# Kernel tuning notes

Measured on AMD Instinct MI355X. Metric: run time of the kernel, lower is better.

## Reference

```python
import jax, jax.numpy as jnp
import numpy as np

N = 2048      # nodes per graph
Q = 9         # output_dim (emotion nodes)
D = 256       # input_dim == hidden_dim
L = 4         # num_layers - 1 GIN layers
B = 32        # batch
E = 32768     # edges per graph
EPS = 1e-5    # BatchNorm eps


def _bn(x, g, b, m, v):
    # eval-mode BatchNorm1d over last (channel) dim
    return (x - m) * (g * jax.lax.rsqrt(v + EPS)) + b


def setup_inputs() -> dict:
    key = jax.random.key(0)
    ks = jax.random.split(key, 18)
    s = 1.0 / np.sqrt(D)
    return {
        "batch_feature": jax.random.normal(ks[0], (B, N, D), jnp.float32),
        "edge_mat": jax.random.randint(ks[1], (2, E), 0, N, dtype=jnp.int32),
        "emotion_emb": jax.random.normal(ks[2], (1, Q, D), jnp.float32) * 0.05,
        "mlp_w1": jax.random.normal(ks[3], (L, D, D), jnp.float32) * s,
        "mlp_b1": jnp.zeros((L, D), jnp.float32),
        "mlp_bn_g": jnp.ones((L, D), jnp.float32),
        "mlp_bn_b": jnp.zeros((L, D), jnp.float32),
        "mlp_bn_m": jax.random.normal(ks[4], (L, D), jnp.float32) * 0.1,
        "mlp_bn_v": jax.random.uniform(ks[5], (L, D), jnp.float32, 0.5, 1.5),
        "mlp_w2": jax.random.normal(ks[6], (L, D, D), jnp.float32) * s,
        "mlp_b2": jnp.zeros((L, D), jnp.float32),
        "bn_g": jnp.ones((L, D), jnp.float32),
        "bn_b": jnp.zeros((L, D), jnp.float32),
        "bn_m": jax.random.normal(ks[7], (L, D), jnp.float32) * 0.1,
        "bn_v": jax.random.uniform(ks[8], (L, D), jnp.float32, 0.5, 1.5),
        "pred_w": jax.random.normal(ks[9], (L + 1, D), jnp.float32) * s,
        "pred_b": jnp.zeros((L + 1,), jnp.float32),
    }


def reference(batch_feature, edge_mat, emotion_emb, mlp_w1, mlp_b1,
              mlp_bn_g, mlp_bn_b, mlp_bn_m, mlp_bn_v, mlp_w2, mlp_b2,
              bn_g, bn_b, bn_m, bn_v, pred_w, pred_b):
    # overwrite first Q node rows with shared emotion embeddings
    h = batch_feature.at[:, :Q, :].set(emotion_emb)          # [B, N, D]
    src, dst = edge_mat[0], edge_mat[1]

    def spmm(x):
        # Adj @ x with self-loops; graph topology shared across batch.
        gathered = x[:, dst, :]                              # [B, E, D]
        agg = jax.vmap(
            lambda g: jax.ops.segment_sum(g, src, num_segments=N)
        )(gathered)                                          # [B, N, D]
        return agg + x  # self-loop (identity added to adjacency)

    hidden = [h]
    for l in range(L):
        pooled = spmm(h)
        # 2-layer GIN MLP: Linear -> BN -> ReLU -> Linear
        t = jnp.einsum('bnd,de->bne', pooled, mlp_w1[l]) + mlp_b1[l]
        t = jax.nn.relu(_bn(t, mlp_bn_g[l], mlp_bn_b[l], mlp_bn_m[l], mlp_bn_v[l]))
        t = jnp.einsum('bnd,de->bne', t, mlp_w2[l]) + mlp_b2[l]
        # outer BatchNorm + ReLU
        h = jax.nn.relu(_bn(t, bn_g[l], bn_b[l], bn_m[l], bn_v[l]))
        hidden.append(h)

    score = jnp.zeros((B, Q), jnp.float32)
    for l, hl in enumerate(hidden):
        h_emotion = hl[:, :Q, :]                             # [B, Q, D]
        score = score + jnp.einsum('bqd,d->bq', h_emotion, pred_w[l]) + pred_b[l]
    return jax.nn.sigmoid(score)                             # [B, Q]
```

## Files before the change

kernel.cpp:

```cpp
#include <hip/hip_runtime.h>
#include <hip/hip_bf16.h>

#define NN 2048
#define QQ 9
#define DD 256
#define LL 4
#define BB 32
#define EE 32768
#define EPSV 1e-5f

typedef __attribute__((ext_vector_type(8))) short bf16x8;
typedef __attribute__((ext_vector_type(8))) ushort u16x8;
typedef __attribute__((ext_vector_type(4))) float f32x4;
typedef __attribute__((ext_vector_type(4))) int i32x4;

__device__ __forceinline__ ushort f2bf(float x)
{
    uint u = __float_as_uint(x);
    u += 0x7FFFu + ((u >> 16) & 1u);
    return (ushort)(u >> 16);
}
__device__ __forceinline__ float bf2f(ushort h)
{
    return __uint_as_float(((uint)h) << 16);
}

__global__ void k_count(const int* __restrict__ src, int* __restrict__ cnt)
{
    int e = blockIdx.x * blockDim.x + threadIdx.x;
    if (e < EE) atomicAdd(&cnt[src[e]], 1);
}

__global__ __launch_bounds__(256) void k_scan(const int* __restrict__ cnt,
                                              int* __restrict__ row_ptr,
                                              int* __restrict__ cursor)
{
    __shared__ int part[256];
    int t = threadIdx.x;
    int local[8];
    int s = 0;
    #pragma unroll
    for (int i = 0; i < 8; ++i) { local[i] = cnt[t * 8 + i]; s += local[i]; }
    part[t] = s;
    __syncthreads();
    for (int off = 1; off < 256; off <<= 1) {
        int v = (t >= off) ? part[t - off] : 0;
        __syncthreads();
        part[t] += v;
        __syncthreads();
    }
    int run = part[t] - s;
    #pragma unroll
    for (int i = 0; i < 8; ++i) {
        int idx = t * 8 + i;
        row_ptr[idx] = run;
        cursor[idx]  = run;
        run += local[i];
    }
    if (t == 255) row_ptr[NN] = run;
}

__global__ void k_fill(const int* __restrict__ src, const int* __restrict__ dst,
                       int* __restrict__ cursor, int* __restrict__ col)
{
    int e = blockIdx.x * blockDim.x + threadIdx.x;
    if (e < EE) {
        int p = atomicAdd(&cursor[src[e]], 1);
        col[p] = dst[e];
    }
}

__global__ void k_prep0(const float4* __restrict__ bf, const float4* __restrict__ emo,
                        ushort4* __restrict__ hhi)
{
    int total = BB * NN * (DD / 4);
    for (int idx = blockIdx.x * blockDim.x + threadIdx.x; idx < total;
         idx += gridDim.x * blockDim.x) {
        int d4 = idx & 63;
        int n  = (idx >> 6) & (NN - 1);
        float4 v = (n < QQ) ? emo[n * 64 + d4] : bf[idx];
        ushort4 h;
        h.x = f2bf(v.x); h.y = f2bf(v.y); h.z = f2bf(v.z); h.w = f2bf(v.w);
        hhi[idx] = h;
    }
}

__global__ __launch_bounds__(256) void k_spmm6(
    const ushort* __restrict__ phi,
    const int* __restrict__ row_ptr, const int* __restrict__ col,
    ushort* __restrict__ ohi)
{
    int x     = blockIdx.x & 7;
    int local = blockIdx.x >> 3;
    int w     = threadIdx.x >> 6;
    int t     = threadIdx.x & 63;
    int inst  = local * 4 + w;
    int pl    = inst >> 11;
    int n     = inst & (NN - 1);
    int b     = x * 4 + pl * 2 + (t >> 5);
    int q     = t & 31;
    const ushort* base = phi + (size_t)b * NN * DD + q * 8;

    u16x8 sv = *(const u16x8*)(base + (size_t)n * DD);
    float a[8];
    #pragma unroll
    for (int k = 0; k < 8; ++k) a[k] = bf2f((ushort)sv[k]);

    int beg = row_ptr[n], end = row_ptr[n + 1];
    int j = beg;
    for (; j < end && (j & 3); ++j) {
        u16x8 g = *(const u16x8*)(base + (size_t)col[j] * DD);
        #pragma unroll
        for (int k = 0; k < 8; ++k) a[k] += bf2f((ushort)g[k]);
    }
    for (; j + 8 <= end; j += 8) {
        i32x4 c0 = *(const i32x4*)(col + j);
        i32x4 c1 = *(const i32x4*)(col + j + 4);
        u16x8 g[8];
        g[0] = *(const u16x8*)(base + (size_t)c0.x * DD);
        g[1] = *(const u16x8*)(base + (size_t)c0.y * DD);
        g[2] = *(const u16x8*)(base + (size_t)c0.z * DD);
        g[3] = *(const u16x8*)(base + (size_t)c0.w * DD);
        g[4] = *(const u16x8*)(base + (size_t)c1.x * DD);
        g[5] = *(const u16x8*)(base + (size_t)c1.y * DD);
        g[6] = *(const u16x8*)(base + (size_t)c1.z * DD);
        g[7] = *(const u16x8*)(base + (size_t)c1.w * DD);
        #pragma unroll
        for (int u = 0; u < 8; ++u)
            #pragma unroll
            for (int k = 0; k < 8; ++k) a[k] += bf2f((ushort)g[u][k]);
    }
    if (j + 4 <= end) {
        i32x4 c = *(const i32x4*)(col + j);
        u16x8 g[4];
        g[0] = *(const u16x8*)(base + (size_t)c.x * DD);
        g[1] = *(const u16x8*)(base + (size_t)c.y * DD);
        g[2] = *(const u16x8*)(base + (size_t)c.z * DD);
        g[3] = *(const u16x8*)(base + (size_t)c.w * DD);
        #pragma unroll
        for (int u = 0; u < 4; ++u)
            #pragma unroll
            for (int k = 0; k < 8; ++k) a[k] += bf2f((ushort)g[u][k]);
        j += 4;
    }
    for (; j < end; ++j) {
        u16x8 g = *(const u16x8*)(base + (size_t)col[j] * DD);
        #pragma unroll
        for (int k = 0; k < 8; ++k) a[k] += bf2f((ushort)g[k]);
    }

    u16x8 o;
    #pragma unroll
    for (int k = 0; k < 8; ++k) o[k] = f2bf(a[k]);
    *(u16x8*)(ohi + ((size_t)b * NN + n) * DD + q * 8) = o;
}

__global__ __launch_bounds__(256) void k_wprep(const float* __restrict__ w1,
                                               const float* __restrict__ w2,
                                               ushort* __restrict__ wt_hi)
{
    __shared__ float tile[32][36];
    int bx = blockIdx.x;
    int mat = bx >> 6;
    int tt  = bx & 63;
    int tk = (tt >> 3) * 32;
    int tn = (tt & 7) * 32;
    const float* src = (mat < 4) ? (w1 + (size_t)mat * DD * DD)
                                 : (w2 + (size_t)(mat - 4) * DD * DD);
    int t = threadIdx.x;
    int r = t >> 3, c0 = (t & 7) * 4;
    float4 v = *(const float4*)(src + (size_t)(tk + r) * DD + tn + c0);
    tile[r][c0 + 0] = v.x; tile[r][c0 + 1] = v.y;
    tile[r][c0 + 2] = v.z; tile[r][c0 + 3] = v.w;
    __syncthreads();
    int nn = t >> 3, kq = (t & 7) * 4;
    ushort4 hh;
    hh.x = f2bf(tile[kq + 0][nn]); hh.y = f2bf(tile[kq + 1][nn]);
    hh.z = f2bf(tile[kq + 2][nn]); hh.w = f2bf(tile[kq + 3][nn]);
    size_t off = (size_t)mat * DD * DD + (size_t)(tn + nn) * DD + tk + kq;
    *(ushort4*)(wt_hi + off) = hh;
}

__global__ __launch_bounds__(256, 2) void k_gemm_fused(
    const ushort* __restrict__ A, const ushort* __restrict__ W1t,
    const ushort* __restrict__ W2t,
    const float* __restrict__ b1, const float* __restrict__ g1,
    const float* __restrict__ be1, const float* __restrict__ m1,
    const float* __restrict__ v1,
    const float* __restrict__ b2, const float* __restrict__ g2,
    const float* __restrict__ be2, const float* __restrict__ m2,
    const float* __restrict__ v2,
    const float* __restrict__ pw, const float* __restrict__ pb, int l,
    ushort* __restrict__ O, float* __restrict__ out)
{
    __shared__ alignas(16) ushort As[2][64 * 32];
    __shared__ alignas(16) ushort Ws[2][256 * 32];
    __shared__ alignas(16) ushort Ts[64][264];

    int tid = threadIdx.x;
    int x  = blockIdx.x & 7;
    int lm = blockIdx.x >> 3;
    int m0 = x * 8192 + lm * 64;
    int lane = tid & 63;
    int w = tid >> 6;
    int wm = w & 1, wn = w >> 1;
    int lr = lane & 15, kg = lane >> 4;
    int rg = lane >> 4;

    int ar = tid >> 2, ak = (tid & 3) * 8;
    const ushort* Ab = A + (size_t)(m0 + ar) * DD + ak;

    f32x4 acc[2][8];
    #pragma unroll
    for (int m = 0; m < 2; ++m)
        #pragma unroll
        for (int n = 0; n < 8; ++n) acc[m][n] = (f32x4)0.f;

    float4 rA;
    float4 rW[4];
    rA = *(const float4*)(Ab);
    #pragma unroll
    for (int i = 0; i < 4; ++i) {
        int idx = tid + i * 256;
        int r = idx >> 2, k8 = (idx & 3) * 8;
        rW[i] = *(const float4*)(W1t + (size_t)r * DD + k8);
    }
    int cur = 0;
    for (int kc = 0; kc < 8; ++kc) {
        *(float4*)&As[cur][ar * 32 + ak] = rA;
        #pragma unroll
        for (int i = 0; i < 4; ++i) {
            int idx = tid + i * 256;
            int r = idx >> 2, k8 = (idx & 3) * 8;
            *(float4*)&Ws[cur][r * 32 + k8] = rW[i];
        }
        __syncthreads();
        if (kc < 7) {
            int k0n = (kc + 1) * 32;
            rA = *(const float4*)(Ab + k0n);
            #pragma unroll
            for (int i = 0; i < 4; ++i) {
                int idx = tid + i * 256;
                int r = idx >> 2, k8 = (idx & 3) * 8;
                rW[i] = *(const float4*)(W1t + (size_t)r * DD + k0n + k8);
            }
        }
        bf16x8 ah[2], bh[8];
        #pragma unroll
        for (int m = 0; m < 2; ++m)
            ah[m] = *(const bf16x8*)&As[cur][(wm * 32 + m * 16 + lr) * 32 + kg * 8];
        #pragma unroll
        for (int n = 0; n < 8; ++n)
            bh[n] = *(const bf16x8*)&Ws[cur][(wn * 128 + n * 16 + lr) * 32 + kg * 8];
        #pragma unroll
        for (int m = 0; m < 2; ++m)
            #pragma unroll
            for (int n = 0; n < 8; ++n)
                acc[m][n] = __builtin_amdgcn_mfma_f32_16x16x32_bf16(ah[m], bh[n], acc[m][n], 0, 0, 0);
        cur ^= 1;
    }
    {
        float sN[8], svN[8];
        #pragma unroll
        for (int n = 0; n < 8; ++n) {
            int jj = wn * 128 + n * 16 + lr;
            sN[n]  = g1[jj] * rsqrtf(v1[jj] + EPSV);
            svN[n] = (b1[jj] - m1[jj]) * sN[n] + be1[jj];
        }
        #pragma unroll
        for (int m = 0; m < 2; ++m)
            #pragma unroll
            for (int n = 0; n < 8; ++n) {
                int cc = wn * 128 + n * 16 + lr;
                #pragma unroll
                for (int r = 0; r < 4; ++r) {
                    float y = acc[m][n][r] * sN[n] + svN[n];
                    Ts[wm * 32 + m * 16 + rg * 4 + r][cc] = f2bf(y > 0.f ? y : 0.f);
                }
            }
    }
    #pragma unroll
    for (int m = 0; m < 2; ++m)
        #pragma unroll
        for (int n = 0; n < 8; ++n) acc[m][n] = (f32x4)0.f;

    __syncthreads();

    #pragma unroll
    for (int i = 0; i < 4; ++i) {
        int idx = tid + i * 256;
        int r = idx >> 2, k8 = (idx & 3) * 8;
        rW[i] = *(const float4*)(W2t + (size_t)r * DD + k8);
    }
    cur = 0;
    for (int kc = 0; kc < 8; ++kc) {
        #pragma unroll
        for (int i = 0; i < 4; ++i) {
            int idx = tid + i * 256;
            int r = idx >> 2, k8 = (idx & 3) * 8;
            *(float4*)&Ws[cur][r * 32 + k8] = rW[i];
        }
        __syncthreads();
        if (kc < 7) {
            int k0n = (kc + 1) * 32;
            #pragma unroll
            for (int i = 0; i < 4; ++i) {
                int idx = tid + i * 256;
                int r = idx >> 2, k8 = (idx & 3) * 8;
                rW[i] = *(const float4*)(W2t + (size_t)r * DD + k0n + k8);
            }
        }
        bf16x8 ah[2], bh[8];
        #pragma unroll
        for (int m = 0; m < 2; ++m)
            ah[m] = *(const bf16x8*)&Ts[wm * 32 + m * 16 + lr][kc * 32 + kg * 8];
        #pragma unroll
        for (int n = 0; n < 8; ++n)
            bh[n] = *(const bf16x8*)&Ws[cur][(wn * 128 + n * 16 + lr) * 32 + kg * 8];
        #pragma unroll
        for (int m = 0; m < 2; ++m)
            #pragma unroll
            for (int n = 0; n < 8; ++n)
                acc[m][n] = __builtin_amdgcn_mfma_f32_16x16x32_bf16(ah[m], bh[n], acc[m][n], 0, 0, 0);
        cur ^= 1;
    }
    __syncthreads();

    {
        float sN[8], svN[8];
        #pragma unroll
        for (int n = 0; n < 8; ++n) {
            int jj = wn * 128 + n * 16 + lr;
            sN[n]  = g2[jj] * rsqrtf(v2[jj] + EPSV);
            svN[n] = (b2[jj] - m2[jj]) * sN[n] + be2[jj];
        }
        #pragma unroll
        for (int m = 0; m < 2; ++m)
            #pragma unroll
            for (int n = 0; n < 8; ++n) {
                int cc = wn * 128 + n * 16 + lr;
                #pragma unroll
                for (int r = 0; r < 4; ++r) {
                    float y = acc[m][n][r] * sN[n] + svN[n];
                    Ts[wm * 32 + m * 16 + rg * 4 + r][cc] = f2bf(y > 0.f ? y : 0.f);
                }
            }
        #pragma unroll
        for (int i = 0; i < 8; ++i) {
            int cid = lane + i * 64;
            int row = cid >> 4, c8 = cid & 15;
            u16x8 vv = *(const u16x8*)&Ts[wm * 32 + row][wn * 128 + c8 * 8];
            *(u16x8*)(O + (size_t)(m0 + wm * 32 + row) * DD + wn * 128 + c8 * 8) = vv;
        }
    }

    __syncthreads();
    if ((m0 & (NN - 1)) == 0) {
        int b = m0 >> 11;
        for (int q = w; q < QQ; q += 4) {
            ushort4 hv = *(const ushort4*)&Ts[q][lane * 4];
            const float4 wv = *(const float4*)&pw[(l + 1) * DD + lane * 4];
            float s = bf2f(hv.x) * wv.x + bf2f(hv.y) * wv.y +
                      bf2f(hv.z) * wv.z + bf2f(hv.w) * wv.w;
            #pragma unroll
            for (int off = 32; off > 0; off >>= 1) s += __shfl_down(s, off);
            if (lane == 0) {
                float v = out[b * QQ + q] + s + pb[l + 1];
                out[b * QQ + q] = (l == LL - 1) ? 1.f / (1.f + expf(-v)) : v;
            }
        }
    }
}

__global__ __launch_bounds__(64) void k_score0(const float4* __restrict__ emo,
                                               const float4* __restrict__ pw,
                                               const float* __restrict__ pb,
                                               float* __restrict__ out)
{
    int q = blockIdx.x, t = threadIdx.x;
    float4 e = emo[q * 64 + t], wv = pw[t];
    float s = e.x * wv.x + e.y * wv.y + e.z * wv.z + e.w * wv.w;
    #pragma unroll
    for (int off = 32; off > 0; off >>= 1) s += __shfl_down(s, off);
    if (t == 0) {
        s += pb[0];
        for (int b = 0; b < BB; ++b) out[b * QQ + q] = s;
    }
}

extern "C" void kernel_launch(void* const* d_in, const int* in_sizes, int n_in,
                              void* d_out, int out_size, void* d_ws, size_t ws_size,
                              hipStream_t stream)
{
    const float* batch = (const float*)d_in[0];
    const int*   edges = (const int*)d_in[1];
    const float* emo   = (const float*)d_in[2];
    const float* w1    = (const float*)d_in[3];
    const float* b1    = (const float*)d_in[4];
    const float* m_g   = (const float*)d_in[5];
    const float* m_b   = (const float*)d_in[6];
    const float* m_m   = (const float*)d_in[7];
    const float* m_v   = (const float*)d_in[8];
    const float* w2    = (const float*)d_in[9];
    const float* b2    = (const float*)d_in[10];
    const float* g_g   = (const float*)d_in[11];
    const float* g_b   = (const float*)d_in[12];
    const float* g_m   = (const float*)d_in[13];
    const float* g_v   = (const float*)d_in[14];
    const float* pw    = (const float*)d_in[15];
    const float* pb    = (const float*)d_in[16];
    float* out = (float*)d_out;

    const size_t HSZ = (size_t)BB * NN * DD;
    const size_t WT  = (size_t)8 * DD * DD;

    ushort* h_hi = (ushort*)d_ws;
    ushort* P_hi = h_hi + HSZ;
    ushort* wt_hi = P_hi + HSZ;
    int* cnt     = (int*)(wt_hi + WT);
    int* row_ptr = cnt + NN;
    int* cursor  = row_ptr + (NN + 4);
    int* col     = cursor + NN;

    const int* src = edges;
    const int* dst = edges + EE;

    hipMemsetAsync(cnt, 0, NN * sizeof(int), stream);
    k_count<<<EE / 256, 256, 0, stream>>>(src, cnt);
    k_scan<<<1, 256, 0, stream>>>(cnt, row_ptr, cursor);
    k_fill<<<EE / 256, 256, 0, stream>>>(src, dst, cursor, col);
    k_wprep<<<512, 256, 0, stream>>>(w1, w2, wt_hi);
    k_prep0<<<4096, 256, 0, stream>>>((const float4*)batch, (const float4*)emo,
                                      (ushort4*)h_hi);
    k_score0<<<QQ, 64, 0, stream>>>((const float4*)emo, (const float4*)pw, pb, out);

    for (int l = 0; l < LL; ++l) {
        k_spmm6<<<8192, 256, 0, stream>>>(h_hi, row_ptr, col, P_hi);
        k_gemm_fused<<<1024, 256, 0, stream>>>(
            P_hi,
            wt_hi + (size_t)l * DD * DD, wt_hi + (size_t)(4 + l) * DD * DD,
            b1 + l * DD, m_g + l * DD, m_b + l * DD, m_m + l * DD, m_v + l * DD,
            b2 + l * DD, g_g + l * DD, g_b + l * DD, g_m + l * DD, g_v + l * DD,
            pw, pb, l,
            h_hi, out);
    }
}
```

Measured before the change: 316.7 us.

## Load GEMM operands directly from global into MFMA registers, dropping LDS staging

The fused two-GEMM kernel no longer stages A and weight tiles through double-buffered shared memory. Each wave now loads its MFMA fragments straight from global memory into register double buffers, which removes the per-k-step __syncthreads and the LDS writes and reads. In exchange, each weight tile is fetched separately by every wave that needs it instead of once per block, so L2/global traffic rises. Register pressure also grows, and the launch-bounds occupancy hint of 2 is dropped.

```diff
diff --git a/kernel.cpp b/kernel.cpp
--- a/kernel.cpp
+++ b/kernel.cpp
@@ -181,7 +181,7 @@
     *(ushort4*)(wt_hi + off) = hh;
 }
 
-__global__ __launch_bounds__(256, 2) void k_gemm_fused(
+__global__ __launch_bounds__(256) void k_gemm_fused(
     const ushort* __restrict__ A, const ushort* __restrict__ W1t,
     const ushort* __restrict__ W2t,
     const float* __restrict__ b1, const float* __restrict__ g1,
@@ -193,8 +193,6 @@
     const float* __restrict__ pw, const float* __restrict__ pb, int l,
     ushort* __restrict__ O, float* __restrict__ out)
 {
-    __shared__ alignas(16) ushort As[2][64 * 32];
-    __shared__ alignas(16) ushort Ws[2][256 * 32];
     __shared__ alignas(16) ushort Ts[64][264];
 
     int tid = threadIdx.x;
@@ -207,57 +205,36 @@
     int lr = lane & 15, kg = lane >> 4;
     int rg = lane >> 4;
 
-    int ar = tid >> 2, ak = (tid & 3) * 8;
-    const ushort* Ab = A + (size_t)(m0 + ar) * DD + ak;
-
     f32x4 acc[2][8];
     #pragma unroll
     for (int m = 0; m < 2; ++m)
         #pragma unroll
         for (int n = 0; n < 8; ++n) acc[m][n] = (f32x4)0.f;
 
-    float4 rA;
-    float4 rW[4];
-    rA = *(const float4*)(Ab);
-    #pragma unroll
-    for (int i = 0; i < 4; ++i) {
-        int idx = tid + i * 256;
-        int r = idx >> 2, k8 = (idx & 3) * 8;
-        rW[i] = *(const float4*)(W1t + (size_t)r * DD + k8);
-    }
-    int cur = 0;
+    const ushort* Ab = A + (size_t)(m0 + wm * 32 + lr) * DD + kg * 8;
+    const ushort* Wb = W1t + (size_t)(wn * 128 + lr) * DD + kg * 8;
+    bf16x8 aa[2][2], bb[2][8];
+    #pragma unroll
+    for (int mi = 0; mi < 2; ++mi) aa[0][mi] = *(const bf16x8*)(Ab + mi * 16 * DD);
+    #pragma unroll
+    for (int n = 0; n < 8; ++n)    bb[0][n]  = *(const bf16x8*)(Wb + n * 16 * DD);
+    #pragma unroll
     for (int kc = 0; kc < 8; ++kc) {
-        *(float4*)&As[cur][ar * 32 + ak] = rA;
-        #pragma unroll
-        for (int i = 0; i < 4; ++i) {
-            int idx = tid + i * 256;
-            int r = idx >> 2, k8 = (idx & 3) * 8;
-            *(float4*)&Ws[cur][r * 32 + k8] = rW[i];
-        }
-        __syncthreads();
+        const int cb = kc & 1, nb = cb ^ 1;
         if (kc < 7) {
-            int k0n = (kc + 1) * 32;
-            rA = *(const float4*)(Ab + k0n);
-            #pragma unroll
-            for (int i = 0; i < 4; ++i) {
-                int idx = tid + i * 256;
-                int r = idx >> 2, k8 = (idx & 3) * 8;
-                rW[i] = *(const float4*)(W1t + (size_t)r * DD + k0n + k8);
-            }
-        }
-        bf16x8 ah[2], bh[8];
-        #pragma unroll
-        for (int m = 0; m < 2; ++m)
-            ah[m] = *(const bf16x8*)&As[cur][(wm * 32 + m * 16 + lr) * 32 + kg * 8];
-        #pragma unroll
-        for (int n = 0; n < 8; ++n)
-            bh[n] = *(const bf16x8*)&Ws[cur][(wn * 128 + n * 16 + lr) * 32 + kg * 8];
-        #pragma unroll
-        for (int m = 0; m < 2; ++m)
+            #pragma unroll
+            for (int mi = 0; mi < 2; ++mi)
+                aa[nb][mi] = *(const bf16x8*)(Ab + mi * 16 * DD + (kc + 1) * 32);
             #pragma unroll
             for (int n = 0; n < 8; ++n)
-                acc[m][n] = __builtin_amdgcn_mfma_f32_16x16x32_bf16(ah[m], bh[n], acc[m][n], 0, 0, 0);
-        cur ^= 1;
+                bb[nb][n] = *(const bf16x8*)(Wb + n * 16 * DD + (kc + 1) * 32);
+        }
+        #pragma unroll
+        for (int mi = 0; mi < 2; ++mi)
+            #pragma unroll
+            for (int n = 0; n < 8; ++n)
+                acc[mi][n] = __builtin_amdgcn_mfma_f32_16x16x32_bf16(
+                    aa[cb][mi], bb[cb][n], acc[mi][n], 0, 0, 0);
     }
     {
         float sN[8], svN[8];
@@ -286,43 +263,27 @@
 
     __syncthreads();
 
-    #pragma unroll
-    for (int i = 0; i < 4; ++i) {
-        int idx = tid + i * 256;
-        int r = idx >> 2, k8 = (idx & 3) * 8;
-        rW[i] = *(const float4*)(W2t + (size_t)r * DD + k8);
-    }
-    cur = 0;
+    Wb = W2t + (size_t)(wn * 128 + lr) * DD + kg * 8;
+    #pragma unroll
+    for (int n = 0; n < 8; ++n) bb[0][n] = *(const bf16x8*)(Wb + n * 16 * DD);
+    #pragma unroll
     for (int kc = 0; kc < 8; ++kc) {
-        #pragma unroll
-        for (int i = 0; i < 4; ++i) {
-            int idx = tid + i * 256;
-            int r = idx >> 2, k8 = (idx & 3) * 8;
-            *(float4*)&Ws[cur][r * 32 + k8] = rW[i];
-        }
-        __syncthreads();
+        const int cb = kc & 1, nb = cb ^ 1;
         if (kc < 7) {
-            int k0n = (kc + 1) * 32;
-            #pragma unroll
-            for (int i = 0; i < 4; ++i) {
-                int idx = tid + i * 256;
-                int r = idx >> 2, k8 = (idx & 3) * 8;
-                rW[i] = *(const float4*)(W2t + (size_t)r * DD + k0n + k8);
-            }
-        }
-        bf16x8 ah[2], bh[8];
-        #pragma unroll
-        for (int m = 0; m < 2; ++m)
-            ah[m] = *(const bf16x8*)&Ts[wm * 32 + m * 16 + lr][kc * 32 + kg * 8];
-        #pragma unroll
-        for (int n = 0; n < 8; ++n)
-            bh[n] = *(const bf16x8*)&Ws[cur][(wn * 128 + n * 16 + lr) * 32 + kg * 8];
-        #pragma unroll
-        for (int m = 0; m < 2; ++m)
             #pragma unroll
             for (int n = 0; n < 8; ++n)
-                acc[m][n] = __builtin_amdgcn_mfma_f32_16x16x32_bf16(ah[m], bh[n], acc[m][n], 0, 0, 0);
-        cur ^= 1;
+                bb[nb][n] = *(const bf16x8*)(Wb + n * 16 * DD + (kc + 1) * 32);
+        }
+        bf16x8 a2[2];
+        #pragma unroll
+        for (int mi = 0; mi < 2; ++mi)
+            a2[mi] = *(const bf16x8*)&Ts[wm * 32 + mi * 16 + lr][kc * 32 + kg * 8];
+        #pragma unroll
+        for (int mi = 0; mi < 2; ++mi)
+            #pragma unroll
+            for (int n = 0; n < 8; ++n)
+                acc[mi][n] = __builtin_amdgcn_mfma_f32_16x16x32_bf16(
+                    a2[mi], bb[cb][n], acc[mi][n], 0, 0, 0);
     }
     __syncthreads();
 
```

After: 470.2 us. 48.5% more time.
